# Kernel optimization log

Hardware: AMD Instinct MI355X
Metric: run time of the kernel (lower is better)

The kernel has to match this reference:

```python
import jax, jax.numpy as jnp
import numpy as np

B, L, C = 256, 168, 36   # batch, length, sensor channels
F = 64                   # number_filter
D = 256                  # token_d_model
DIV = 3                  # div_sa
STEP = L // DIV          # 56 chunks (L divisible by DIV)


def setup_inputs() -> dict:
    key = jax.random.key(0)
    ks = jax.random.split(key, 16)
    inp = {}
    inp["x"] = jax.random.normal(ks[0], (B, L, C), jnp.float32)
    # conv2d stack: kernel (5,1), padding same, with bias
    inp["w0"] = jax.random.normal(ks[1], (F, 1, 5, 1), jnp.float32) * (1.0 / np.sqrt(5))
    inp["b0"] = jnp.zeros((F,), jnp.float32)
    for i in range(1, 4):
        inp[f"w{i}"] = jax.random.normal(ks[1 + i], (F, F, 5, 1), jnp.float32) * (1.0 / np.sqrt(5 * F))
        inp[f"b{i}"] = jnp.zeros((F,), jnp.float32)
    # self-attention 1x1 conv1d projections (no bias): (F*DIV -> F)
    s = 1.0 / np.sqrt(DIV * F)
    inp["wq"] = jax.random.normal(ks[5], (F, DIV * F), jnp.float32) * s
    inp["wk"] = jax.random.normal(ks[6], (F, DIV * F), jnp.float32) * s
    inp["wv"] = jax.random.normal(ks[7], (F, DIV * F), jnp.float32) * s
    inp["wv1"] = jax.random.normal(ks[8], (F, DIV * F), jnp.float32) * s
    inp["gamma"] = jnp.zeros((1,), jnp.float32)
    # fc: Linear(F*C -> D)
    inp["fc_w"] = jax.random.normal(ks[9], (D, F * C), jnp.float32) * (1.0 / np.sqrt(F * C))
    inp["fc_b"] = jnp.zeros((D,), jnp.float32)
    return inp


def _conv2d_same(x, w, b):
    y = jax.lax.conv_general_dilated(
        x, w, window_strides=(1, 1), padding="SAME",
        dimension_numbers=("NCHW", "OIHW", "NCHW"))
    return y + b[None, :, None, None]


def reference(x, w0, b0, w1, b1, w2, b2, w3, b3, wq, wk, wv, wv1, gamma, fc_w, fc_b):
    h = x[:, None, :, :]  # (B,1,L,C)
    for w, b in ((w0, b0), (w1, b1), (w2, b2), (w3, b3)):
        h = jax.nn.relu(_conv2d_same(h, w, b))  # (B,F,L,C)
    # chunk the length dim into STEP blocks of DIV rows, flatten F-major: (B,STEP,F*DIV,C)
    xc = h.reshape(B, F, STEP, DIV, C).transpose(0, 2, 1, 3, 4).reshape(B, STEP, F * DIV, C)
    # 1x1 conv1d projections == matmul over the F*DIV axis
    f = jnp.einsum("qk,bskc->bsqc", wq, xc)    # (B,STEP,F,C)
    g = jnp.einsum("qk,bskc->bsqc", wk, xc)
    hv = jnp.einsum("qk,bskc->bsqc", wv, xc)
    v1 = jnp.einsum("qk,bskc->bsqc", wv1, xc)
    # scores[b,s,i,j] = sum_q f[...,i] g[...,j]; torch softmax(dim=1) of (B,C,C) -> axis i
    scores = jnp.einsum("bsqi,bsqj->bsij", f, g)  # (B,STEP,C,C)
    beta = jax.nn.softmax(scores, axis=2)
    o = gamma[0] * jnp.einsum("bsqi,bsij->bsqj", hv, beta) + v1  # (B,STEP,F,C)
    # cat chunks along last dim then permute(0,3,1,2) == (B,STEP,F,C) already
    o = jax.nn.relu(o).reshape(B, STEP, F * C)
    # dropout is identity in eval mode
    out = jax.nn.relu(o @ fc_w.T + fc_b)  # (B,STEP,D)
    return out
```

## Files before the change

kernel.cpp:

```cpp
#include <hip/hip_runtime.h>
#include <hip/hip_bf16.h>

#define BB   256
#define LL   168
#define CC   36
#define FF   64
#define SSTEP 56

typedef __attribute__((ext_vector_type(8))) _Float16 half8;
typedef __attribute__((ext_vector_type(4))) _Float16 half4;
typedef __attribute__((ext_vector_type(4))) float f32x4;

#define MFMA16(a,b,c) __builtin_amdgcn_mfma_f32_16x16x32_f16(a,b,c,0,0,0)

__global__ __launch_bounds__(256) void k0_prep(
    const float* __restrict__ w1, const float* __restrict__ w2, const float* __restrict__ w3,
    const float* __restrict__ wq, const float* __restrict__ wk,
    const float* __restrict__ wv, const float* __restrict__ wv1,
    const float* __restrict__ fcw,
    _Float16* __restrict__ wcb, _Float16* __restrict__ pwb, _Float16* __restrict__ fcB)
{
    const int N1 = 61440;
    const int N2 = 49152;
    const int N3 = 589824;
    int idx = blockIdx.x * 256 + threadIdx.x;
    if (idx < N1) {
        int lin = idx;
        int j    = lin & 7;   lin >>= 3;
        int lane = lin & 63;  lin >>= 6;
        int mt   = lin & 3;   lin >>= 2;
        int t    = lin % 5;   lin /= 5;
        int kk   = lin & 1;
        int layer = lin >> 1;
        int fo = mt * 16 + (lane & 15);
        int fi = kk * 32 + (lane >> 4) * 8 + j;
        const float* w = (layer == 0) ? w1 : (layer == 1) ? w2 : w3;
        wcb[idx] = (_Float16)w[fo * 320 + fi * 5 + t];
    } else if (idx < N1 + N2) {
        int e = idx - N1;
        int p = e / 12288, r = e % 12288;
        int kkp = r / 2048, r2 = r % 2048;
        int wv_ = r2 / 512, r3 = r2 % 512;
        int lane = r3 / 8, j = r3 % 8;
        int q  = wv_ * 16 + (lane & 15);
        int kp = kkp * 32 + (lane >> 4) * 8 + j;
        int d  = kp >> 6, f = kp & 63;
        const float* w = (p == 0) ? wq : (p == 1) ? wk : (p == 2) ? wv : wv1;
        pwb[e] = (_Float16)w[q * 192 + f * 3 + d];
    } else if (idx < N1 + N2 + N3) {
        int e = idx - N1 - N2;
        int d = e / 2304, kc = e % 2304;
        int cc = kc >> 6, q = kc & 63;
        fcB[e] = (_Float16)fcw[d * 2304 + q * 36 + cc];
    }
}

__global__ __launch_bounds__(256, 4) void k1_conv_proj(
    const float* __restrict__ x,
    const float* __restrict__ w0, const float* __restrict__ cb0,
    const float* __restrict__ cb1, const float* __restrict__ cb2,
    const float* __restrict__ cb3,
    const _Float16* __restrict__ wcb,
    const _Float16* __restrict__ pwb,
    const float* __restrict__ gamma,
    _Float16* __restrict__ P,
    _Float16* __restrict__ O,
    int b_start)
{
    __shared__ int4 hbv[1440];
    __shared__ float xl[176];
    char* hb  = (char*)hbv;
    const int tid  = threadIdx.x;
    const int lane = tid & 63, wid = tid >> 6;
    const int c = blockIdx.x % CC, bl = blockIdx.x / CC, b = b_start + bl;
    const float gam = gamma[0];
    const int4 IZ = make_int4(0, 0, 0, 0);
    const f32x4 FZ = {0.f, 0.f, 0.f, 0.f};
    const int pfirst = (gam == 0.f) ? 3 : 0;

    if (tid < 16) hbv[tid] = IZ;
    if (tid >= 32 && tid < 112) hbv[1328 + tid] = IZ;
    if (tid < 176) {
        int l = tid - 2;
        xl[tid] = (l >= 0 && l < LL) ? x[((size_t)b * LL + l) * CC + c] : 0.f;
    }
    __syncthreads();

    {
        float wt0 = w0[lane*5], wt1 = w0[lane*5+1], wt2 = w0[lane*5+2],
              wt3 = w0[lane*5+3], wt4 = w0[lane*5+4];
        float bb = cb0[lane];
        const int l0 = wid * 42;
        float h0 = xl[l0], h1 = xl[l0+1], h2 = xl[l0+2], h3 = xl[l0+3];
        #pragma unroll 6
        for (int i = 0; i < 42; ++i) {
            float h4 = xl[l0 + i + 4];
            float a = bb + wt0*h0 + wt1*h1 + wt2*h2 + wt3*h3 + wt4*h4;
            int row = l0 + i + 2;
            *(_Float16*)(hb + row*128 + ((lane*2) ^ ((row&7)<<4))) = (_Float16)fmaxf(a, 0.f);
            h0 = h1; h1 = h2; h2 = h3; h3 = h4;
        }
    }
    __syncthreads();

    const int fo = lane & 15;
    const int g8 = (lane >> 4) << 4;

    #pragma unroll 1
    for (int layer = 0; layer < 3; ++layer) {
        const float* bias = (layer == 0) ? cb1 : (layer == 1) ? cb2 : cb3;
        f32x4 acc[4][3];
        #pragma unroll
        for (int mt = 0; mt < 4; ++mt)
            #pragma unroll
            for (int i = 0; i < 3; ++i) acc[mt][i] = FZ;

        #pragma unroll
        for (int kk = 0; kk < 2; ++kk) {
            const _Float16* wb = wcb + layer*20480 + kk*10240 + lane*8;
            const int cb = kk*64 + g8;
            #pragma unroll
            for (int t = 0; t < 5; ++t) {
                half8 a0 = *(const half8*)(wb + t*2048 + 0*512);
                half8 a1 = *(const half8*)(wb + t*2048 + 1*512);
                half8 a2 = *(const half8*)(wb + t*2048 + 2*512);
                half8 a3 = *(const half8*)(wb + t*2048 + 3*512);
                #pragma unroll
                for (int i = 0; i < 3; ++i) {
                    const int nt = wid + 4*i;
                    if (nt < 11) {
                        int row = nt*16 + fo + t;
                        half8 bf = *(const half8*)(hb + row*128 + (cb ^ ((row&7)<<4)));
                        acc[0][i] = MFMA16(a0, bf, acc[0][i]);
                        acc[1][i] = MFMA16(a1, bf, acc[1][i]);
                        acc[2][i] = MFMA16(a2, bf, acc[2][i]);
                        acc[3][i] = MFMA16(a3, bf, acc[3][i]);
                    }
                }
            }
        }
        __syncthreads();

        if (layer < 2) {
            #pragma unroll
            for (int mt = 0; mt < 4; ++mt) {
                const int fo0 = mt*16 + ((lane>>4)<<2);
                const float bb0 = bias[fo0], bb1 = bias[fo0+1],
                            bb2 = bias[fo0+2], bb3 = bias[fo0+3];
                #pragma unroll
                for (int i = 0; i < 3; ++i) {
                    const int nt = wid + 4*i;
                    const int l  = nt*16 + fo;
                    if (nt < 11 && l < LL) {
                        int row = l + 2;
                        half4 hv;
                        hv.x = (_Float16)fmaxf(acc[mt][i].x + bb0, 0.f);
                        hv.y = (_Float16)fmaxf(acc[mt][i].y + bb1, 0.f);
                        hv.z = (_Float16)fmaxf(acc[mt][i].z + bb2, 0.f);
                        hv.w = (_Float16)fmaxf(acc[mt][i].w + bb3, 0.f);
                        *(half4*)(hb + row*128 + ((fo0*2) ^ ((row&7)<<4))) = hv;
                    }
                }
            }
        } else {
            #pragma unroll
            for (int mt = 0; mt < 4; ++mt) {
                const int fo0 = mt*16 + ((lane>>4)<<2);
                const float bb0 = bias[fo0], bb1 = bias[fo0+1],
                            bb2 = bias[fo0+2], bb3 = bias[fo0+3];
                #pragma unroll
                for (int i = 0; i < 3; ++i) {
                    const int nt = wid + 4*i;
                    const int l  = nt*16 + fo;
                    if (nt < 11 && l < LL) {
                        const int s = l / 3, d = l - s*3;
                        const int ssw = (s & 7) << 4;
                        half4 hv;
                        hv.x = (_Float16)fmaxf(acc[mt][i].x + bb0, 0.f);
                        hv.y = (_Float16)fmaxf(acc[mt][i].y + bb1, 0.f);
                        hv.z = (_Float16)fmaxf(acc[mt][i].z + bb2, 0.f);
                        hv.w = (_Float16)fmaxf(acc[mt][i].w + bb3, 0.f);
                        *(half4*)(hb + s*384 + ((d*128 + fo0*2) ^ ssw)) = hv;
                    }
                }
            }
        }
        __syncthreads();
    }

    const half8 HZ = {(_Float16)0,(_Float16)0,(_Float16)0,(_Float16)0,
                      (_Float16)0,(_Float16)0,(_Float16)0,(_Float16)0};
    #pragma unroll 1
    for (int p = pfirst; p < 4; ++p) {
        f32x4 pacc[4] = {FZ, FZ, FZ, FZ};
        const _Float16* ab = pwb + p*12288 + wid*512 + lane*8;
        #pragma unroll
        for (int kkp = 0; kkp < 6; ++kkp) {
            half8 af = *(const half8*)(ab + kkp*2048);
            const int cb = kkp*64 + g8;
            #pragma unroll
            for (int nt = 0; nt < 4; ++nt) {
                const int s = nt*16 + fo;
                half8 bf = HZ;
                if (s < SSTEP)
                    bf = *(const half8*)(hb + s*384 + (cb ^ ((s&7)<<4)));
                pacc[nt] = MFMA16(af, bf, pacc[nt]);
            }
        }
        const int q0 = wid*16 + ((lane>>4)<<2);
        #pragma unroll
        for (int nt = 0; nt < 4; ++nt) {
            const int s = nt*16 + fo;
            if (s >= SSTEP) continue;
            const size_t bs = (size_t)bl * SSTEP + s;
            half4 o;
            if (p == 3 && gam == 0.f) {
                o.x = (_Float16)fmaxf(pacc[nt].x, 0.f);
                o.y = (_Float16)fmaxf(pacc[nt].y, 0.f);
                o.z = (_Float16)fmaxf(pacc[nt].z, 0.f);
                o.w = (_Float16)fmaxf(pacc[nt].w, 0.f);
                *(half4*)(O + bs*2304 + c*64 + q0) = o;
            } else {
                o.x = (_Float16)pacc[nt].x;
                o.y = (_Float16)pacc[nt].y;
                o.z = (_Float16)pacc[nt].z;
                o.w = (_Float16)pacc[nt].w;
                *(half4*)(P + (bs*4 + p)*2304 + c*64 + q0) = o;
            }
        }
    }
}

__global__ __launch_bounds__(256) void k2_attn(
    const _Float16* __restrict__ P,
    const float* __restrict__ gamma,
    _Float16* __restrict__ O)
{
    const float gam = gamma[0];
    if (gam == 0.f) return;
    const int bs  = blockIdx.x;
    const int tid = threadIdx.x;
    __shared__ float pb[4][CC][FF];
    __shared__ float sc[CC][CC];

    const size_t base = (size_t)bs * 4 * 2304;
    for (int idx = tid; idx < 4 * 2304; idx += 256)
        ((float*)pb)[idx] = (float)P[base + idx];
    __syncthreads();

    for (int idx = tid; idx < CC * CC; idx += 256) {
        int i = idx / CC, jj = idx % CC;
        float a = 0.f;
        for (int qq = 0; qq < FF; ++qq) a += pb[0][i][qq] * pb[1][jj][qq];
        sc[i][jj] = a;
    }
    __syncthreads();
    if (tid < CC) {
        int jj = tid;
        float m = -1e30f;
        for (int i = 0; i < CC; ++i) m = fmaxf(m, sc[i][jj]);
        float ssum = 0.f;
        for (int i = 0; i < CC; ++i) ssum += expf(sc[i][jj] - m);
        float inv = 1.f / ssum;
        for (int i = 0; i < CC; ++i) sc[i][jj] = expf(sc[i][jj] - m) * inv;
    }
    __syncthreads();

    for (int idx = tid; idx < FF * CC; idx += 256) {
        int qq = idx / CC, jj = idx % CC;
        float a = 0.f;
        for (int i = 0; i < CC; ++i) a += pb[2][i][qq] * sc[i][jj];
        float o = gam * a + pb[3][jj][qq];
        O[(size_t)bs * 2304 + jj * 64 + qq] = (_Float16)fmaxf(o, 0.f);
    }
}

__global__ __launch_bounds__(256) void k3_fc(
    const _Float16* __restrict__ O,
    const _Float16* __restrict__ fcB,
    const float* __restrict__ fcb,
    float* __restrict__ out,
    int rows, int gm)
{
    const int bm = blockIdx.x % gm, bn = blockIdx.x / gm;
    const int r0 = bm * 64, c0 = bn * 64;
    const int tid = threadIdx.x, lane = tid & 63, wid = tid >> 6;
    __shared__ _Float16 As[64][40];
    __shared__ _Float16 Bs[64][40];

    const f32x4 FZ = {0.f, 0.f, 0.f, 0.f};
    f32x4 acc[4] = {FZ, FZ, FZ, FZ};
    const int rr = tid >> 2, k8 = (tid & 3) * 8;
    const int4 IZ = make_int4(0, 0, 0, 0);

    for (int k0 = 0; k0 < 2304; k0 += 32) {
        __syncthreads();
        int4 av = (r0 + rr < rows)
            ? *(const int4*)(O + (size_t)(r0 + rr) * 2304 + k0 + k8) : IZ;
        *(int4*)&As[rr][k8] = av;
        *(int4*)&Bs[rr][k8] = *(const int4*)(fcB + (size_t)(c0 + rr) * 2304 + k0 + k8);
        __syncthreads();
        const int cb = (lane >> 4) << 4;
        half8 af = *(const half8*)((char*)As + (wid*16 + (lane & 15)) * 80 + cb);
        #pragma unroll
        for (int ct = 0; ct < 4; ++ct) {
            half8 bf = *(const half8*)((char*)Bs + (ct*16 + (lane & 15)) * 80 + cb);
            acc[ct] = MFMA16(af, bf, acc[ct]);
        }
    }
    #pragma unroll
    for (int ct = 0; ct < 4; ++ct) {
        const int d = c0 + ct*16 + (lane & 15);
        const float bb = fcb[d];
        #pragma unroll
        for (int r = 0; r < 4; ++r) {
            const int row = r0 + wid*16 + ((lane>>4)<<2) + r;
            if (row < rows) out[(size_t)row * 256 + d] = fmaxf(acc[ct][r] + bb, 0.f);
        }
    }
}

extern "C" void kernel_launch(void* const* d_in, const int* in_sizes, int n_in,
                              void* d_out, int out_size, void* d_ws, size_t ws_size,
                              hipStream_t stream)
{
    const float* x     = (const float*)d_in[0];
    const float* w0    = (const float*)d_in[1];
    const float* b0    = (const float*)d_in[2];
    const float* w1    = (const float*)d_in[3];
    const float* b1    = (const float*)d_in[4];
    const float* w2    = (const float*)d_in[5];
    const float* b2    = (const float*)d_in[6];
    const float* w3    = (const float*)d_in[7];
    const float* b3    = (const float*)d_in[8];
    const float* wq    = (const float*)d_in[9];
    const float* wk    = (const float*)d_in[10];
    const float* wv    = (const float*)d_in[11];
    const float* wv1   = (const float*)d_in[12];
    const float* gamma = (const float*)d_in[13];
    const float* fcw   = (const float*)d_in[14];
    const float* fcb   = (const float*)d_in[15];
    float* out = (float*)d_out;

    const size_t fixedB = (size_t)(61440 + 49152 + 589824) * 2;
    const size_t perB   = (size_t)SSTEP * 4 * 2304 * 2 + (size_t)SSTEP * 2304 * 2;
    int Bc = 256;
    while (Bc > 1 && fixedB + (size_t)Bc * perB > ws_size) Bc >>= 1;

    char* ws = (char*)d_ws;
    _Float16* wcb = (_Float16*)ws;
    _Float16* pwb = wcb + 61440;
    _Float16* fcB = pwb + 49152;
    _Float16* P   = (_Float16*)(ws + fixedB);
    _Float16* O   = P + (size_t)Bc * SSTEP * 4 * 2304;

    const int prep_total = 61440 + 49152 + 589824;
    k0_prep<<<(prep_total + 255) / 256, 256, 0, stream>>>(w1, w2, w3, wq, wk, wv, wv1,
                                                          fcw, wcb, pwb, fcB);

    for (int bst = 0; bst < BB; bst += Bc) {
        int bcur = (bst + Bc <= BB) ? Bc : (BB - bst);
        k1_conv_proj<<<bcur * CC, 256, 0, stream>>>(x, w0, b0, b1, b2, b3,
                                                    wcb, pwb, gamma, P, O, bst);
        k2_attn<<<bcur * SSTEP, 256, 0, stream>>>(P, gamma, O);
        int rows = bcur * SSTEP;
        int gm = (rows + 63) / 64;
        k3_fc<<<gm * 4, 256, 0, stream>>>(O, fcB, fcb,
                                          out + (size_t)bst * SSTEP * 256, rows, gm);
    }
}
```

Baseline: 352.0 us.

## Split conv/projection kernel along length into two halves with halo recompute

Each k1 block now handles half the sequence (84 rows plus an 8-row halo on each side) instead of all 168 rows, which doubles the grid size and shrinks shared memory per block. Warps are remapped to a 2x2 split over filters and positions, and the projection works on 28 chunks per block. The launch bound rises from 4 to 6 waves to raise occupancy. The cost is recomputing the halo rows through the four conv layers and a tighter register budget.

```diff
diff --git a/kernel.cpp b/kernel.cpp
--- a/kernel.cpp
+++ b/kernel.cpp
@@ -55,7 +55,7 @@
     }
 }
 
-__global__ __launch_bounds__(256, 4) void k1_conv_proj(
+__global__ __launch_bounds__(256, 6) void k1_conv_proj(
     const float* __restrict__ x,
     const float* __restrict__ w0, const float* __restrict__ cb0,
     const float* __restrict__ cb1, const float* __restrict__ cb2,
@@ -67,75 +67,79 @@
     _Float16* __restrict__ O,
     int b_start)
 {
-    __shared__ int4 hbv[1440];
-    __shared__ float xl[176];
+    __shared__ int4 hbv[832];
+    __shared__ float xl[104];
     char* hb  = (char*)hbv;
     const int tid  = threadIdx.x;
     const int lane = tid & 63, wid = tid >> 6;
-    const int c = blockIdx.x % CC, bl = blockIdx.x / CC, b = b_start + bl;
+    const int bx = blockIdx.x;
+    const int c = bx % CC;
+    const int r0b = bx / CC;
+    const int half = r0b & 1;
+    const int bl = r0b >> 1;
+    const int b = b_start + bl;
+    const int L0 = half * 84;
     const float gam = gamma[0];
     const int4 IZ = make_int4(0, 0, 0, 0);
     const f32x4 FZ = {0.f, 0.f, 0.f, 0.f};
     const int pfirst = (gam == 0.f) ? 3 : 0;
 
-    if (tid < 16) hbv[tid] = IZ;
-    if (tid >= 32 && tid < 112) hbv[1328 + tid] = IZ;
-    if (tid < 176) {
-        int l = tid - 2;
+    for (int i = tid; i < 832; i += 256) hbv[i] = IZ;
+    if (tid < 104) {
+        int l = L0 + tid - 8;
         xl[tid] = (l >= 0 && l < LL) ? x[((size_t)b * LL + l) * CC + c] : 0.f;
     }
     __syncthreads();
+
+    const int c15 = lane & 15;
+    const int g   = lane >> 4;
+    const int g8  = g << 4;
+    const int m2  = wid & 1;
+    const int n3  = wid >> 1;
 
     {
         float wt0 = w0[lane*5], wt1 = w0[lane*5+1], wt2 = w0[lane*5+2],
               wt3 = w0[lane*5+3], wt4 = w0[lane*5+4];
         float bb = cb0[lane];
-        const int l0 = wid * 42;
-        float h0 = xl[l0], h1 = xl[l0+1], h2 = xl[l0+2], h3 = xl[l0+3];
+        const int rr0 = 2 + wid * 24;
+        float h0 = xl[rr0-2], h1 = xl[rr0-1], h2 = xl[rr0], h3 = xl[rr0+1];
         #pragma unroll 6
-        for (int i = 0; i < 42; ++i) {
-            float h4 = xl[l0 + i + 4];
+        for (int i = 0; i < 24; ++i) {
+            int rr = rr0 + i;
+            float h4 = xl[rr + 2];
             float a = bb + wt0*h0 + wt1*h1 + wt2*h2 + wt3*h3 + wt4*h4;
-            int row = l0 + i + 2;
-            *(_Float16*)(hb + row*128 + ((lane*2) ^ ((row&7)<<4))) = (_Float16)fmaxf(a, 0.f);
+            int l = L0 + rr - 8;
+            if (l >= 0 && l < LL)
+                *(_Float16*)(hb + rr*128 + ((lane*2) ^ ((rr&7)<<4))) = (_Float16)fmaxf(a, 0.f);
             h0 = h1; h1 = h2; h2 = h3; h3 = h4;
         }
     }
     __syncthreads();
-
-    const int fo = lane & 15;
-    const int g8 = (lane >> 4) << 4;
 
     #pragma unroll 1
     for (int layer = 0; layer < 3; ++layer) {
         const float* bias = (layer == 0) ? cb1 : (layer == 1) ? cb2 : cb3;
-        f32x4 acc[4][3];
-        #pragma unroll
-        for (int mt = 0; mt < 4; ++mt)
-            #pragma unroll
-            for (int i = 0; i < 3; ++i) acc[mt][i] = FZ;
+        f32x4 acc[2][3];
+        #pragma unroll
+        for (int j = 0; j < 2; ++j)
+            #pragma unroll
+            for (int i = 0; i < 3; ++i) acc[j][i] = FZ;
 
         #pragma unroll
         for (int kk = 0; kk < 2; ++kk) {
-            const _Float16* wb = wcb + layer*20480 + kk*10240 + lane*8;
+            const _Float16* wb = wcb + layer*20480 + kk*10240 + m2*1024 + lane*8;
             const int cb = kk*64 + g8;
             #pragma unroll
             for (int t = 0; t < 5; ++t) {
-                half8 a0 = *(const half8*)(wb + t*2048 + 0*512);
-                half8 a1 = *(const half8*)(wb + t*2048 + 1*512);
-                half8 a2 = *(const half8*)(wb + t*2048 + 2*512);
-                half8 a3 = *(const half8*)(wb + t*2048 + 3*512);
+                half8 a0 = *(const half8*)(wb + t*2048);
+                half8 a1 = *(const half8*)(wb + t*2048 + 512);
                 #pragma unroll
                 for (int i = 0; i < 3; ++i) {
-                    const int nt = wid + 4*i;
-                    if (nt < 11) {
-                        int row = nt*16 + fo + t;
-                        half8 bf = *(const half8*)(hb + row*128 + (cb ^ ((row&7)<<4)));
-                        acc[0][i] = MFMA16(a0, bf, acc[0][i]);
-                        acc[1][i] = MFMA16(a1, bf, acc[1][i]);
-                        acc[2][i] = MFMA16(a2, bf, acc[2][i]);
-                        acc[3][i] = MFMA16(a3, bf, acc[3][i]);
-                    }
+                    const int nt = n3*3 + i;
+                    int row = nt*16 + c15 + t;
+                    half8 bf = *(const half8*)(hb + row*128 + (cb ^ ((row&7)<<4)));
+                    acc[0][i] = MFMA16(a0, bf, acc[0][i]);
+                    acc[1][i] = MFMA16(a1, bf, acc[1][i]);
                 }
             }
         }
@@ -143,43 +147,44 @@
 
         if (layer < 2) {
             #pragma unroll
-            for (int mt = 0; mt < 4; ++mt) {
-                const int fo0 = mt*16 + ((lane>>4)<<2);
+            for (int j = 0; j < 2; ++j) {
+                const int fo0 = (m2*2 + j)*16 + (g<<2);
                 const float bb0 = bias[fo0], bb1 = bias[fo0+1],
                             bb2 = bias[fo0+2], bb3 = bias[fo0+3];
                 #pragma unroll
                 for (int i = 0; i < 3; ++i) {
-                    const int nt = wid + 4*i;
-                    const int l  = nt*16 + fo;
-                    if (nt < 11 && l < LL) {
-                        int row = l + 2;
+                    const int nt = n3*3 + i;
+                    const int ro = 2 + nt*16 + c15;
+                    const int l  = L0 + ro - 8;
+                    if (l >= 0 && l < LL) {
                         half4 hv;
-                        hv.x = (_Float16)fmaxf(acc[mt][i].x + bb0, 0.f);
-                        hv.y = (_Float16)fmaxf(acc[mt][i].y + bb1, 0.f);
-                        hv.z = (_Float16)fmaxf(acc[mt][i].z + bb2, 0.f);
-                        hv.w = (_Float16)fmaxf(acc[mt][i].w + bb3, 0.f);
-                        *(half4*)(hb + row*128 + ((fo0*2) ^ ((row&7)<<4))) = hv;
+                        hv.x = (_Float16)fmaxf(acc[j][i].x + bb0, 0.f);
+                        hv.y = (_Float16)fmaxf(acc[j][i].y + bb1, 0.f);
+                        hv.z = (_Float16)fmaxf(acc[j][i].z + bb2, 0.f);
+                        hv.w = (_Float16)fmaxf(acc[j][i].w + bb3, 0.f);
+                        *(half4*)(hb + ro*128 + ((fo0*2) ^ ((ro&7)<<4))) = hv;
                     }
                 }
             }
         } else {
             #pragma unroll
-            for (int mt = 0; mt < 4; ++mt) {
-                const int fo0 = mt*16 + ((lane>>4)<<2);
+            for (int j = 0; j < 2; ++j) {
+                const int fo0 = (m2*2 + j)*16 + (g<<2);
                 const float bb0 = bias[fo0], bb1 = bias[fo0+1],
                             bb2 = bias[fo0+2], bb3 = bias[fo0+3];
                 #pragma unroll
                 for (int i = 0; i < 3; ++i) {
-                    const int nt = wid + 4*i;
-                    const int l  = nt*16 + fo;
-                    if (nt < 11 && l < LL) {
-                        const int s = l / 3, d = l - s*3;
+                    const int nt = n3*3 + i;
+                    const int ro = 2 + nt*16 + c15;
+                    const int rl = ro - 8;
+                    if (rl >= 0 && rl < 84) {
+                        const int s = rl / 3, d = rl - s*3;
                         const int ssw = (s & 7) << 4;
                         half4 hv;
-                        hv.x = (_Float16)fmaxf(acc[mt][i].x + bb0, 0.f);
-                        hv.y = (_Float16)fmaxf(acc[mt][i].y + bb1, 0.f);
-                        hv.z = (_Float16)fmaxf(acc[mt][i].z + bb2, 0.f);
-                        hv.w = (_Float16)fmaxf(acc[mt][i].w + bb3, 0.f);
+                        hv.x = (_Float16)fmaxf(acc[j][i].x + bb0, 0.f);
+                        hv.y = (_Float16)fmaxf(acc[j][i].y + bb1, 0.f);
+                        hv.z = (_Float16)fmaxf(acc[j][i].z + bb2, 0.f);
+                        hv.w = (_Float16)fmaxf(acc[j][i].w + bb3, 0.f);
                         *(half4*)(hb + s*384 + ((d*128 + fo0*2) ^ ssw)) = hv;
                     }
                 }
@@ -192,27 +197,27 @@
                       (_Float16)0,(_Float16)0,(_Float16)0,(_Float16)0};
     #pragma unroll 1
     for (int p = pfirst; p < 4; ++p) {
-        f32x4 pacc[4] = {FZ, FZ, FZ, FZ};
+        f32x4 pacc[2] = {FZ, FZ};
         const _Float16* ab = pwb + p*12288 + wid*512 + lane*8;
         #pragma unroll
         for (int kkp = 0; kkp < 6; ++kkp) {
             half8 af = *(const half8*)(ab + kkp*2048);
             const int cb = kkp*64 + g8;
             #pragma unroll
-            for (int nt = 0; nt < 4; ++nt) {
-                const int s = nt*16 + fo;
+            for (int nt = 0; nt < 2; ++nt) {
+                const int sl = nt*16 + c15;
                 half8 bf = HZ;
-                if (s < SSTEP)
-                    bf = *(const half8*)(hb + s*384 + (cb ^ ((s&7)<<4)));
+                if (sl < 28)
+                    bf = *(const half8*)(hb + sl*384 + (cb ^ ((sl&7)<<4)));
                 pacc[nt] = MFMA16(af, bf, pacc[nt]);
             }
         }
-        const int q0 = wid*16 + ((lane>>4)<<2);
-        #pragma unroll
-        for (int nt = 0; nt < 4; ++nt) {
-            const int s = nt*16 + fo;
-            if (s >= SSTEP) continue;
-            const size_t bs = (size_t)bl * SSTEP + s;
+        const int q0 = wid*16 + (g<<2);
+        #pragma unroll
+        for (int nt = 0; nt < 2; ++nt) {
+            const int sl = nt*16 + c15;
+            if (sl >= 28) continue;
+            const size_t bs = (size_t)bl * SSTEP + half*28 + sl;
             half4 o;
             if (p == 3 && gam == 0.f) {
                 o.x = (_Float16)fmaxf(pacc[nt].x, 0.f);
@@ -360,8 +365,8 @@
 
     for (int bst = 0; bst < BB; bst += Bc) {
         int bcur = (bst + Bc <= BB) ? Bc : (BB - bst);
-        k1_conv_proj<<<bcur * CC, 256, 0, stream>>>(x, w0, b0, b1, b2, b3,
-                                                    wcb, pwb, gamma, P, O, bst);
+        k1_conv_proj<<<bcur * CC * 2, 256, 0, stream>>>(x, w0, b0, b1, b2, b3,
+                                                        wcb, pwb, gamma, P, O, bst);
         k2_attn<<<bcur * SSTEP, 256, 0, stream>>>(P, gamma, O);
         int rows = bcur * SSTEP;
         int gm = (rows + 63) / 64;
```

Measured after the change: 438.6 us. +24.6%, slower.
